# Performance work log

Measured on AMD Instinct MI355X. Metric: run time of the kernel, lower is better.

The kernel has to match this reference:

```python
import jax, jax.numpy as jnp
import numpy as np

SEQ, B, IN, HID = 512, 64, 1024, 1024


def setup_inputs() -> dict:
    key = jax.random.key(0)
    ks = jax.random.split(key, 9)
    scale = 1.0 / np.sqrt(IN + HID)  # ~torch Linear init range
    def lin(k):
        kw, kb = jax.random.split(k)
        W = jax.random.uniform(kw, (IN + HID, HID), jnp.float32, -scale, scale)
        b = jax.random.uniform(kb, (HID,), jnp.float32, -scale, scale)
        return W, b
    W_f, b_f = lin(ks[0])
    W_i, b_i = lin(ks[1])
    W_o, b_o = lin(ks[2])
    W_c, b_c = lin(ks[3])
    x = jax.random.normal(ks[4], (SEQ, B, IN), jnp.float32)
    return {"x": x, "W_f": W_f, "b_f": b_f, "W_i": W_i, "b_i": b_i,
            "W_o": W_o, "b_o": b_o, "W_c": W_c, "b_c": b_c}


def reference(x, W_f, b_f, W_i, b_i, W_o, b_o, W_c, b_c):
    # x: [seq, batch, input_size]; z = concat(hidden, x_t) to match torch.cat((hidden, input[j]), 1)
    batch = x.shape[1]
    hid = W_f.shape[1]
    h0 = jnp.zeros((batch, hid), x.dtype)
    c0 = jnp.zeros((batch, hid), x.dtype)

    def step(carry, xt):
        h, c = carry
        z = jnp.concatenate([h, xt], axis=1)          # [B, hid+in]
        f = jax.nn.sigmoid(z @ W_f + b_f)
        i = jax.nn.sigmoid(z @ W_i + b_i)
        o = jax.nn.sigmoid(z @ W_o + b_o)
        C_hat = jnp.tanh(z @ W_c + b_c)
        c = c * f + C_hat * i
        h = jnp.tanh(c) * o
        return (h, c), h

    (h, c), output = jax.lax.scan(step, (h0, c0), x)  # output: [seq, B, hid]
    return output, h, c
```

## Files before the change

kernel.cpp:

```cpp
#include <hip/hip_runtime.h>
#include <hip/hip_bf16.h>


typedef __attribute__((ext_vector_type(8))) short short8;
typedef __attribute__((ext_vector_type(4))) float f32x4;
typedef __attribute__((ext_vector_type(4))) unsigned int u32x4;

#define SEQ  512
#define NBAT 64
#define RING 128

static __device__ __forceinline__ unsigned short f2b(float f) {
  unsigned u = __float_as_uint(f);
  unsigned r = (u + 0x7fffu + ((u >> 16) & 1u)) >> 16;
  return (unsigned short)r;
}

static __device__ __forceinline__ void gld_lds16(const void* g, void* l) {
  __builtin_amdgcn_global_load_lds((const __attribute__((address_space(1))) void*)g,
                                   (__attribute__((address_space(3))) void*)l, 16, 0, 0);
}
static __device__ __forceinline__ void gld_lds16_sc1(const void* g, void* l) {
  __builtin_amdgcn_global_load_lds((const __attribute__((address_space(1))) void*)g,
                                   (__attribute__((address_space(3))) void*)l, 16, 0, 16);
}

static __device__ __forceinline__ float sigf(float x) { return 1.f / (1.f + __expf(-x)); }
static __device__ __forceinline__ float tanhfast(float x) { return 1.f - 2.f / (1.f + __expf(2.f * x)); }


__global__ __launch_bounds__(512) void pack_w(const float* __restrict__ Wf,
                                              const float* __restrict__ Wi,
                                              const float* __restrict__ Wo,
                                              const float* __restrict__ Wc,
                                              unsigned short* __restrict__ Wht,
                                              unsigned short* __restrict__ Wxt) {
  __shared__ float tile[64][65];
  int bx = blockIdx.x;
  int g  = bx & 3; bx >>= 2;
  int jb = bx & 15;
  int kb = bx >> 4;
  int j0 = jb * 64, k0 = kb * 64;
  const float* W = (g == 0) ? Wf : (g == 1) ? Wi : (g == 2) ? Wo : Wc;
  int t = threadIdx.x;
  {
    int r  = t >> 3;
    int c0 = (t & 7) * 8;
    const float* src = W + (size_t)(k0 + r) * 1024 + j0 + c0;
    float4 a = *(const float4*)src;
    float4 b = *(const float4*)(src + 4);
    tile[r][c0 + 0] = a.x; tile[r][c0 + 1] = a.y; tile[r][c0 + 2] = a.z; tile[r][c0 + 3] = a.w;
    tile[r][c0 + 4] = b.x; tile[r][c0 + 5] = b.y; tile[r][c0 + 6] = b.z; tile[r][c0 + 7] = b.w;
  }
  __syncthreads();
  {
    int jj  = t >> 3;
    int cc8 = t & 7;
    unsigned short v[8];
#pragma unroll
    for (int e = 0; e < 8; ++e) v[e] = f2b(tile[cc8 * 8 + e][jj]);
    size_t p = (size_t)(4 * (j0 + jj) + g);
    if (k0 < 1024)
      *(uint4*)(&Wht[p * 1024 + k0 + cc8 * 8]) = *(const uint4*)v;
    else
      *(uint4*)(&Wxt[p * 1024 + (k0 - 1024) + cc8 * 8]) = *(const uint4*)v;
  }
}

__global__ __launch_bounds__(256) void pack_bias(const float* __restrict__ bf,
                                                 const float* __restrict__ bi,
                                                 const float* __restrict__ bo,
                                                 const float* __restrict__ bc,
                                                 float* __restrict__ bp) {
  int p = blockIdx.x * 256 + threadIdx.x;
  if (p < 4096) {
    int j = p >> 2, g = p & 3;
    const float* b = (g == 0) ? bf : (g == 1) ? bi : (g == 2) ? bo : bc;
    bp[p] = b[j];
  }
}

__global__ __launch_bounds__(256) void conv_x(const float* __restrict__ x,
                                              unsigned short* __restrict__ xb, int n8) {
  int i = blockIdx.x * 256 + threadIdx.x;
  if (i < n8) {
    const float4* xp = (const float4*)x + (size_t)i * 2;
    float4 a = xp[0], b = xp[1];
    unsigned short v[8] = {f2b(a.x), f2b(a.y), f2b(a.z), f2b(a.w),
                           f2b(b.x), f2b(b.y), f2b(b.z), f2b(b.w)};
    *(uint4*)(&xb[(size_t)i * 8]) = *(const uint4*)v;
  }
}

__global__ __launch_bounds__(256) void init_state(unsigned short* __restrict__ hA,
                                                  float* __restrict__ c,
                                                  int* __restrict__ flags,
                                                  int* __restrict__ gxcnt) {
  int i = blockIdx.x * 256 + threadIdx.x;
  if (i < NBAT * 1024) { hA[i] = 0; c[i] = 0.f; }
  if (i < 128) flags[i] = 0;
  if (i < 256) gxcnt[i] = 0;
}


__global__ __launch_bounds__(256, 1) void lstm_fused(
    const unsigned short* __restrict__ Wht,
    const unsigned short* __restrict__ Wxt,
    const float* __restrict__ bp,
    const unsigned short* __restrict__ xb,
    float* __restrict__ GxRing,
    unsigned short* __restrict__ hA,
    unsigned short* __restrict__ hB,
    float* __restrict__ cst,
    float* __restrict__ out,
    float* __restrict__ outH,
    float* __restrict__ outC,
    int* __restrict__ flags,
    int* __restrict__ gxcnt) {
  __shared__ __align__(16) char lds[139584];

  const int tid = threadIdx.x;
  const int bid = blockIdx.x;
  const int lane = tid & 63;

  if (bid < 128) {
    unsigned short* Ws = (unsigned short*)lds;
    char*           Ab = lds + 65536;
    float (*G)[33]     = (float(*)[33])(lds + 131072);
    int* tok           = (int*)(lds + 139520);

    const int w   = tid >> 6;
    const int w16 = w * 16;
    const int rl  = lane & 15;
    const int kb  = lane >> 4;
    const int p0  = bid * 32;

    {
      const unsigned short* Wsrc = Wht + (size_t)p0 * 1024;
#pragma unroll
      for (int r = 0; r < 16; ++r) {
        int s = r * 256 + tid;
        int row = s >> 7;
        int slot = s & 127;
        int sub = (slot & 7) ^ (row & 7);
        gld_lds16(Wsrc + (size_t)row * 1024 + ((slot & ~7) | sub) * 8,
                  Ws + (size_t)(r * 256 + (tid & 192)) * 8);
      }
    }

    const int gb   = tid >> 2;
    const int gjl  = (tid & 3) * 2;
    const int gidx = gb * 1024 + (p0 >> 2) + gjl;
    float c0 = cst[gidx], c1 = cst[gidx + 1];

    if (tid == 0) *tok = 0;
    asm volatile("s_waitcnt vmcnt(0)" ::: "memory");
    __syncthreads();

#define ASTAGE(c_)                                                             \
    {                                                                          \
      const unsigned short* hrow = hsrc + (size_t)w16 * 1024 + (c_) * 128;     \
      char* dbase = Ab + ((c_) & 3) * 16384 + w * 4096;                        \
      _Pragma("unroll") for (int i = 0; i < 4; ++i) {                          \
        int s = i * 64 + lane;                                                 \
        int row_loc = s >> 4;                                                  \
        int slot = s & 15;                                                     \
        int src = slot ^ (row_loc & 7);                                        \
        gld_lds16_sc1(hrow + (size_t)row_loc * 1024 + src * 8,                 \
                      dbase + i * 1024);                                       \
      }                                                                        \
    }

    for (int t = 0; t < SEQ; ++t) {
      const unsigned short* hsrc = (t & 1) ? hB : hA;
      unsigned int*         hdst = (unsigned int*)((t & 1) ? hA : hB);

      if (w == 0) {
        int cready = __hip_atomic_load(&gxcnt[t >> 1], __ATOMIC_RELAXED, __HIP_MEMORY_SCOPE_AGENT);
        if (t > 0) {
          while (true) {
            int m0 = __hip_atomic_load(&flags[lane * 2],     __ATOMIC_RELAXED, __HIP_MEMORY_SCOPE_AGENT);
            int m1 = __hip_atomic_load(&flags[lane * 2 + 1], __ATOMIC_RELAXED, __HIP_MEMORY_SCOPE_AGENT);
            if (__all(m0 >= t && m1 >= t)) break;
            __builtin_amdgcn_s_sleep(1);
          }
        }
        if (cready < 32) {
          while (__hip_atomic_load(&gxcnt[t >> 1], __ATOMIC_RELAXED, __HIP_MEMORY_SCOPE_AGENT) < 32)
            __builtin_amdgcn_s_sleep(2);
        }
        __hip_atomic_store(tok, t + 1, __ATOMIC_RELAXED, __HIP_MEMORY_SCOPE_WORKGROUP);
      } else {
        while (__hip_atomic_load(tok, __ATOMIC_RELAXED, __HIP_MEMORY_SCOPE_WORKGROUP) < t + 1) {
        }
      }
      __builtin_amdgcn_sched_barrier(0);

      u32x4 gxa, gxb;
      {
        const float* gsrc = GxRing + (size_t)(t & (RING - 1)) * 262144 +
                            (size_t)gb * 4096 + p0 + gjl * 4;
        asm volatile("global_load_dwordx4 %0, %1, off sc1" : "=v"(gxa) : "v"(gsrc));
        asm volatile("global_load_dwordx4 %0, %1, off offset:16 sc1" : "=v"(gxb) : "v"(gsrc));
      }
      __builtin_amdgcn_sched_barrier(0);

      ASTAGE(0); ASTAGE(1); ASTAGE(2); ASTAGE(3);

      f32x4 acc0 = (f32x4){0.f, 0.f, 0.f, 0.f};
      f32x4 acc1 = (f32x4){0.f, 0.f, 0.f, 0.f};

#pragma unroll
      for (int kc = 0; kc < 8; ++kc) {
        if      (kc <= 4) asm volatile("s_waitcnt vmcnt(12)" ::: "memory");
        else if (kc == 5) asm volatile("s_waitcnt vmcnt(8)"  ::: "memory");
        else if (kc == 6) asm volatile("s_waitcnt vmcnt(4)"  ::: "memory");
        else              asm volatile("s_waitcnt vmcnt(0)"  ::: "memory");
        __builtin_amdgcn_sched_barrier(0);
        const char* Abc = Ab + (kc & 3) * 16384 + w * 4096;
#pragma unroll
        for (int ks = 0; ks < 4; ++ks) {
          int g = ks * 4 + kb;
          short8 af = *(const short8*)(Abc + rl * 256 + ((g ^ (rl & 7)) * 16));
          int gslot = kc * 16 + g;
          int gbase = (gslot & ~7) * 16;
          short8 bf0 = *(const short8*)((const char*)Ws + (0 * 16 + rl) * 2048 + gbase +
                                        (((gslot & 7) ^ (rl & 7)) * 16));
          short8 bf1 = *(const short8*)((const char*)Ws + (1 * 16 + rl) * 2048 + gbase +
                                        (((gslot & 7) ^ (rl & 7)) * 16));
          acc0 = __builtin_amdgcn_mfma_f32_16x16x32_bf16(af, bf0, acc0, 0, 0, 0);
          acc1 = __builtin_amdgcn_mfma_f32_16x16x32_bf16(af, bf1, acc1, 0, 0, 0);
        }
        if (kc + 4 < 8) ASTAGE(kc + 4);
      }

#pragma unroll
      for (int r = 0; r < 4; ++r) {
        G[w16 + kb * 4 + r][rl]      = acc0[r];
        G[w16 + kb * 4 + r][16 + rl] = acc1[r];
      }
      f32x4 gx0 = __builtin_bit_cast(f32x4, gxa);
      f32x4 gx1 = __builtin_bit_cast(f32x4, gxb);
      float f0 = sigf(G[gb][gjl * 4 + 0] + gx0[0]);
      float i0 = sigf(G[gb][gjl * 4 + 1] + gx0[1]);
      float o0 = sigf(G[gb][gjl * 4 + 2] + gx0[2]);
      float q0 = tanhfast(G[gb][gjl * 4 + 3] + gx0[3]);
      float f1 = sigf(G[gb][gjl * 4 + 4] + gx1[0]);
      float i1 = sigf(G[gb][gjl * 4 + 5] + gx1[1]);
      float o1 = sigf(G[gb][gjl * 4 + 6] + gx1[2]);
      float q1 = tanhfast(G[gb][gjl * 4 + 7] + gx1[3]);
      c0 = c0 * f0 + q0 * i0;
      c1 = c1 * f1 + q1 * i1;
      float h0 = tanhfast(c0) * o0;
      float h1 = tanhfast(c1) * o1;

      __hip_atomic_store(&hdst[gidx >> 1],
                         ((unsigned)f2b(h1) << 16) | (unsigned)f2b(h0),
                         __ATOMIC_RELAXED, __HIP_MEMORY_SCOPE_AGENT);
      asm volatile("s_waitcnt vmcnt(0)" ::: "memory");
      __syncthreads();
      if (tid == 0)
        __hip_atomic_store(&flags[bid], t + 1, __ATOMIC_RELAXED, __HIP_MEMORY_SCOPE_AGENT);

      *(float2*)&out[(size_t)t * 65536 + gidx] = make_float2(h0, h1);
      if (t == SEQ - 1) {
        *(float2*)&outH[gidx] = make_float2(h0, h1);
        *(float2*)&outC[gidx] = make_float2(c0, c1);
      }
    }
#undef ASTAGE

    cst[gidx]     = c0;
    cst[gidx + 1] = c1;

  } else {
    unsigned short* AsW = (unsigned short*)lds;
    unsigned short* BsW = (unsigned short*)(lds + 32768);
    const int wid = bid - 128;
    const int w = tid >> 6;
    const int rl = lane & 15, kb = lane >> 4;
    const int wr = w >> 1, wc = w & 1;

    for (int tau = wid; tau < 8192; tau += 128) {
      int sp = tau >> 5;
      int bn = tau & 31;

      if (2 * sp >= RING - 16) {
        int need = 2 * sp - (RING - 16) + 1;
        while (__hip_atomic_load(&flags[0], __ATOMIC_RELAXED, __HIP_MEMORY_SCOPE_AGENT) < need)
          __builtin_amdgcn_s_sleep(16);
      }

      const unsigned short* Abase = xb + (size_t)sp * 131072;
      const unsigned short* Bbase = Wxt + (size_t)bn * 131072;

      f32x4 acc[4][4];
#pragma unroll
      for (int m = 0; m < 4; ++m)
#pragma unroll
        for (int n = 0; n < 4; ++n) acc[m][n] = (f32x4){0.f, 0.f, 0.f, 0.f};

#define GSTAGE(k0_, buf_)                                                       \
      {                                                                         \
        _Pragma("unroll") for (int r = 0; r < 4; ++r) {                         \
          int i = r * 256 + tid;                                                \
          int row = i >> 3;                                                     \
          int cc = (i & 7) ^ (row & 7);                                         \
          int base = (r * 256 + (tid & 192)) * 8;                               \
          gld_lds16(Abase + (size_t)row * 1024 + (k0_) + cc * 8, &AsW[(buf_)*8192 + base]); \
          gld_lds16(Bbase + (size_t)row * 1024 + (k0_) + cc * 8, &BsW[(buf_)*8192 + base]); \
        }                                                                       \
      }

      GSTAGE(0, 0);
      __syncthreads();
      int cur = 0;
#pragma unroll 2
      for (int kc = 0; kc < 16; ++kc) {
        if (kc < 15) GSTAGE((kc + 1) * 64, cur ^ 1);
        const char* Abt = (const char*)&AsW[cur * 8192];
        const char* Bbt = (const char*)&BsW[cur * 8192];
#pragma unroll
        for (int ks = 0; ks < 2; ++ks) {
          int g = ks * 4 + kb;
          short8 bf[4], af[4];
#pragma unroll
          for (int nt = 0; nt < 4; ++nt) {
            int brow = wc * 64 + nt * 16 + rl;
            bf[nt] = *(const short8*)(Bbt + brow * 128 + ((g ^ (brow & 7)) * 16));
          }
#pragma unroll
          for (int mt = 0; mt < 4; ++mt) {
            int arow = wr * 64 + mt * 16 + rl;
            af[mt] = *(const short8*)(Abt + arow * 128 + ((g ^ (arow & 7)) * 16));
          }
#pragma unroll
          for (int mt = 0; mt < 4; ++mt)
#pragma unroll
            for (int nt = 0; nt < 4; ++nt)
              acc[mt][nt] = __builtin_amdgcn_mfma_f32_16x16x32_bf16(af[mt], bf[nt], acc[mt][nt], 0, 0, 0);
        }
        __syncthreads();
        cur ^= 1;
      }
#undef GSTAGE

      float* Cb = GxRing + (size_t)((2 * sp) & (RING - 1)) * 262144;
#pragma unroll
      for (int nt = 0; nt < 4; ++nt) {
        int p = bn * 128 + wc * 64 + nt * 16 + rl;
        float bias = bp[p];
#pragma unroll
        for (int mt = 0; mt < 4; ++mt) {
#pragma unroll
          for (int r = 0; r < 4; ++r) {
            int row = wr * 64 + mt * 16 + kb * 4 + r;
            __hip_atomic_store(&Cb[(size_t)row * 4096 + p], acc[mt][nt][r] + bias,
                               __ATOMIC_RELAXED, __HIP_MEMORY_SCOPE_AGENT);
          }
        }
      }
      asm volatile("s_waitcnt vmcnt(0)" ::: "memory");
      __syncthreads();
      if (tid == 0)
        __hip_atomic_fetch_add(&gxcnt[sp], 1, __ATOMIC_RELAXED, __HIP_MEMORY_SCOPE_AGENT);
    }
  }
}


extern "C" void kernel_launch(void* const* d_in, const int* in_sizes, int n_in,
                              void* d_out, int out_size, void* d_ws, size_t ws_size,
                              hipStream_t stream) {
  const float* x  = (const float*)d_in[0];
  const float* Wf = (const float*)d_in[1];
  const float* bf = (const float*)d_in[2];
  const float* Wi = (const float*)d_in[3];
  const float* bi = (const float*)d_in[4];
  const float* Wo = (const float*)d_in[5];
  const float* bo = (const float*)d_in[6];
  const float* Wc = (const float*)d_in[7];
  const float* bc = (const float*)d_in[8];
  float* out = (float*)d_out;

  char* ws = (char*)d_ws;
  unsigned short* Wht = (unsigned short*)(ws);
  unsigned short* Wxt = (unsigned short*)(ws + 8388608);
  float*          bp  = (float*)(ws + 16777216);
  unsigned short* xb  = (unsigned short*)(ws + 16793600);
  unsigned short* hA  = (unsigned short*)(ws + 83902464);
  unsigned short* hB  = (unsigned short*)(ws + 84033536);
  float*          cst = (float*)(ws + 84164608);
  int*            flg = (int*)(ws + 84426752);
  int*            gxc = (int*)(ws + 84430848);
  float*          GxR = (float*)(ws + 84440064);

  pack_w    <<<2048,  512, 0, stream>>>(Wf, Wi, Wo, Wc, Wht, Wxt);
  pack_bias <<<16,    256, 0, stream>>>(bf, bi, bo, bc, bp);
  conv_x    <<<16384, 256, 0, stream>>>(x, xb, 4194304);
  init_state<<<256,   256, 0, stream>>>(hA, cst, flg, gxc);

  float* outH = out + (size_t)SEQ * NBAT * 1024;
  float* outC = outH + NBAT * 1024;

  lstm_fused<<<256, 256, 0, stream>>>(Wht, Wxt, bp, xb, GxR, hA, hB, cst,
                                      out, outH, outC, flg, gxc);
}
```

Measured before the change: 3.203 ms.

## Replace flag/counter barriers with sentinel-poisoned data polling in LSTM recurrence

```diff
diff --git a/kernel.cpp b/kernel.cpp
--- a/kernel.cpp
+++ b/kernel.cpp
@@ -8,7 +8,7 @@
 
 #define SEQ  512
 #define NBAT 64
-#define RING 128
+#define RING 32
 
 static __device__ __forceinline__ unsigned short f2b(float f) {
   unsigned u = __float_as_uint(f);
@@ -19,10 +19,6 @@
 static __device__ __forceinline__ void gld_lds16(const void* g, void* l) {
   __builtin_amdgcn_global_load_lds((const __attribute__((address_space(1))) void*)g,
                                    (__attribute__((address_space(3))) void*)l, 16, 0, 0);
-}
-static __device__ __forceinline__ void gld_lds16_sc1(const void* g, void* l) {
-  __builtin_amdgcn_global_load_lds((const __attribute__((address_space(1))) void*)g,
-                                   (__attribute__((address_space(3))) void*)l, 16, 0, 16);
 }
 
 static __device__ __forceinline__ float sigf(float x) { return 1.f / (1.f + __expf(-x)); }
@@ -92,14 +88,19 @@
   }
 }
 
-__global__ __launch_bounds__(256) void init_state(unsigned short* __restrict__ hA,
+__global__ __launch_bounds__(256) void init_state(unsigned int* __restrict__ hR,
                                                   float* __restrict__ c,
-                                                  int* __restrict__ flags,
-                                                  int* __restrict__ gxcnt) {
+                                                  int* __restrict__ flags) {
   int i = blockIdx.x * 256 + threadIdx.x;
-  if (i < NBAT * 1024) { hA[i] = 0; c[i] = 0.f; }
+  if (i < 131072) hR[i] = (i < 98304) ? ~0u : 0u;
+  if (i < 65536) c[i] = 0.f;
   if (i < 128) flags[i] = 0;
-  if (i < 256) gxcnt[i] = 0;
+}
+
+__global__ __launch_bounds__(256) void fill_ring(u32x4* __restrict__ g, int n4) {
+  u32x4 nan4; nan4[0] = ~0u; nan4[1] = ~0u; nan4[2] = ~0u; nan4[3] = ~0u;
+  for (int k = blockIdx.x * 256 + threadIdx.x; k < n4; k += 524288)
+    g[k] = nan4;
 }
 
 
@@ -109,14 +110,12 @@
     const float* __restrict__ bp,
     const unsigned short* __restrict__ xb,
     float* __restrict__ GxRing,
-    unsigned short* __restrict__ hA,
-    unsigned short* __restrict__ hB,
+    unsigned short* __restrict__ hR,
     float* __restrict__ cst,
     float* __restrict__ out,
     float* __restrict__ outH,
     float* __restrict__ outC,
-    int* __restrict__ flags,
-    int* __restrict__ gxcnt) {
+    int* __restrict__ flags) {
   __shared__ __align__(16) char lds[139584];
 
   const int tid = threadIdx.x;
@@ -127,7 +126,6 @@
     unsigned short* Ws = (unsigned short*)lds;
     char*           Ab = lds + 65536;
     float (*G)[33]     = (float(*)[33])(lds + 131072);
-    int* tok           = (int*)(lds + 139520);
 
     const int w   = tid >> 6;
     const int w16 = w * 16;
@@ -153,70 +151,97 @@
     const int gidx = gb * 1024 + (p0 >> 2) + gjl;
     float c0 = cst[gidx], c1 = cst[gidx + 1];
 
-    if (tid == 0) *tok = 0;
     asm volatile("s_waitcnt vmcnt(0)" ::: "memory");
     __syncthreads();
 
-#define ASTAGE(c_)                                                             \
-    {                                                                          \
-      const unsigned short* hrow = hsrc + (size_t)w16 * 1024 + (c_) * 128;     \
-      char* dbase = Ab + ((c_) & 3) * 16384 + w * 4096;                        \
-      _Pragma("unroll") for (int i = 0; i < 4; ++i) {                          \
-        int s = i * 64 + lane;                                                 \
-        int row_loc = s >> 4;                                                  \
-        int slot = s & 15;                                                     \
-        int src = slot ^ (row_loc & 7);                                        \
-        gld_lds16_sc1(hrow + (size_t)row_loc * 1024 + src * 8,                 \
-                      dbase + i * 1024);                                       \
-      }                                                                        \
-    }
+    const int klane = lane >> 4;
+    const int sl    = lane & 15;
+    const int x0 = klane * 2048 + ((sl ^ klane) * 16);
+    const int x1 = (4 + klane) * 2048 + (((sl ^ klane) ^ 4) * 16);
+    const int x2 = x0 + 16384;
+    const int x3 = x1 + 16384;
+    const int wb = w * 32768;
+    char* AbW = Ab + w * 4096 + (size_t)lane * 16;
+
+    const int c_own = bid >> 4;
+    const int ocg   = bid & 15;
+    const int own0  = ((sl ^ klane) == ocg);
+    const int own1  = ((sl ^ (klane + 4)) == ocg);
+    const int row_loc_own = gb - w16;
+    char* ownlds = Ab + (c_own & 3) * 16384 + w * 4096 +
+                   (row_loc_own * 16 + (ocg ^ (row_loc_own & 7))) * 16 + (tid & 3) * 4;
+
+    unsigned hp_prev = 0;
+
+#define HISSUE(c_)                                                             \
+    { const char* cb_ = hbase + (c_) * 256;                                    \
+      asm volatile("global_load_dwordx4 %0, %1, off sc0 sc1"                   \
+                   : "=v"(ch[(c_) & 3][0]) : "v"(cb_ + x0));                   \
+      asm volatile("global_load_dwordx4 %0, %1, off sc0 sc1"                   \
+                   : "=v"(ch[(c_) & 3][1]) : "v"(cb_ + x1));                   \
+      asm volatile("global_load_dwordx4 %0, %1, off sc0 sc1"                   \
+                   : "=v"(ch[(c_) & 3][2]) : "v"(cb_ + x2));                   \
+      asm volatile("global_load_dwordx4 %0, %1, off sc0 sc1"                   \
+                   : "=v"(ch[(c_) & 3][3]) : "v"(cb_ + x3)); }
+
+#define KWAIT(kc_)                                                             \
+    { if ((kc_) <= 4)      asm volatile("s_waitcnt vmcnt(12)" ::: "memory");   \
+      else if ((kc_) == 5) asm volatile("s_waitcnt vmcnt(8)"  ::: "memory");   \
+      else if ((kc_) == 6) asm volatile("s_waitcnt vmcnt(4)"  ::: "memory");   \
+      else                 asm volatile("s_waitcnt vmcnt(0)"  ::: "memory"); }
 
     for (int t = 0; t < SEQ; ++t) {
-      const unsigned short* hsrc = (t & 1) ? hB : hA;
-      unsigned int*         hdst = (unsigned int*)((t & 1) ? hA : hB);
-
-      if (w == 0) {
-        int cready = __hip_atomic_load(&gxcnt[t >> 1], __ATOMIC_RELAXED, __HIP_MEMORY_SCOPE_AGENT);
-        if (t > 0) {
-          while (true) {
-            int m0 = __hip_atomic_load(&flags[lane * 2],     __ATOMIC_RELAXED, __HIP_MEMORY_SCOPE_AGENT);
-            int m1 = __hip_atomic_load(&flags[lane * 2 + 1], __ATOMIC_RELAXED, __HIP_MEMORY_SCOPE_AGENT);
-            if (__all(m0 >= t && m1 >= t)) break;
-            __builtin_amdgcn_s_sleep(1);
-          }
-        }
-        if (cready < 32) {
-          while (__hip_atomic_load(&gxcnt[t >> 1], __ATOMIC_RELAXED, __HIP_MEMORY_SCOPE_AGENT) < 32)
-            __builtin_amdgcn_s_sleep(2);
-        }
-        __hip_atomic_store(tok, t + 1, __ATOMIC_RELAXED, __HIP_MEMORY_SCOPE_WORKGROUP);
-      } else {
-        while (__hip_atomic_load(tok, __ATOMIC_RELAXED, __HIP_MEMORY_SCOPE_WORKGROUP) < t + 1) {
-        }
-      }
+      const char*   hbase = (const char*)hR + ((t + 3) & 3) * 131072 + wb;
+      unsigned int* hdst  = (unsigned int*)((char*)hR + (t & 3) * 131072);
+      unsigned int* hwip  = (unsigned int*)((char*)hR + ((t + 2) & 3) * 131072);
+      float* gsrc = GxRing + (size_t)(t & (RING - 1)) * 262144 +
+                    (size_t)gb * 4096 + p0 + gjl * 4;
+
+      u32x4 gxa, gxb;
+      asm volatile("global_load_dwordx4 %0, %1, off sc0 sc1" : "=v"(gxa) : "v"(gsrc));
+      asm volatile("global_load_dwordx4 %0, %1, off offset:16 sc0 sc1" : "=v"(gxb) : "v"(gsrc));
+      u32x4 ch[4][4];
+      HISSUE(0); HISSUE(1); HISSUE(2); HISSUE(3);
       __builtin_amdgcn_sched_barrier(0);
-
-      u32x4 gxa, gxb;
-      {
-        const float* gsrc = GxRing + (size_t)(t & (RING - 1)) * 262144 +
-                            (size_t)gb * 4096 + p0 + gjl * 4;
-        asm volatile("global_load_dwordx4 %0, %1, off sc1" : "=v"(gxa) : "v"(gsrc));
-        asm volatile("global_load_dwordx4 %0, %1, off offset:16 sc1" : "=v"(gxb) : "v"(gsrc));
-      }
-      __builtin_amdgcn_sched_barrier(0);
-
-      ASTAGE(0); ASTAGE(1); ASTAGE(2); ASTAGE(3);
 
       f32x4 acc0 = (f32x4){0.f, 0.f, 0.f, 0.f};
       f32x4 acc1 = (f32x4){0.f, 0.f, 0.f, 0.f};
 
 #pragma unroll
       for (int kc = 0; kc < 8; ++kc) {
-        if      (kc <= 4) asm volatile("s_waitcnt vmcnt(12)" ::: "memory");
-        else if (kc == 5) asm volatile("s_waitcnt vmcnt(8)"  ::: "memory");
-        else if (kc == 6) asm volatile("s_waitcnt vmcnt(4)"  ::: "memory");
-        else              asm volatile("s_waitcnt vmcnt(0)"  ::: "memory");
+        KWAIT(kc);
         __builtin_amdgcn_sched_barrier(0);
+
+        int rtry = 0;
+        for (;;) {
+          int s0, s1, s2, s3;
+          { u32x4 v = ch[kc & 3][0]; s0 = (v[0]==~0u)|(v[1]==~0u)|(v[2]==~0u)|(v[3]==~0u); }
+          { u32x4 v = ch[kc & 3][1]; s1 = (v[0]==~0u)|(v[1]==~0u)|(v[2]==~0u)|(v[3]==~0u); }
+          { u32x4 v = ch[kc & 3][2]; s2 = (v[0]==~0u)|(v[1]==~0u)|(v[2]==~0u)|(v[3]==~0u); }
+          { u32x4 v = ch[kc & 3][3]; s3 = (v[0]==~0u)|(v[1]==~0u)|(v[2]==~0u)|(v[3]==~0u); }
+          if (kc == c_own) { s0 &= !own0; s1 &= !own1; s2 &= !own0; s3 &= !own1; }
+          if (!__any(s0 | s1 | s2 | s3) || ++rtry > 2048) break;
+          asm volatile("s_waitcnt vmcnt(0)" ::: "memory");
+          __builtin_amdgcn_sched_barrier(0);
+          __builtin_amdgcn_s_sleep(4);
+          HISSUE(kc);
+          asm volatile("s_waitcnt vmcnt(0)" ::: "memory");
+          __builtin_amdgcn_sched_barrier(0);
+        }
+        if (rtry) {
+          if (kc + 1 < 8) HISSUE(kc + 1);
+          if (kc + 2 < 8) HISSUE(kc + 2);
+          if (kc + 3 < 8) HISSUE(kc + 3);
+        }
+
+        { char* wA = AbW + (kc & 3) * 16384;
+          *(u32x4*)(wA)          = ch[kc & 3][0];
+          *(u32x4*)(wA + 1024)   = ch[kc & 3][1];
+          *(u32x4*)(wA + 2048)   = ch[kc & 3][2];
+          *(u32x4*)(wA + 3072)   = ch[kc & 3][3]; }
+        if (kc == c_own) *(unsigned*)ownlds = hp_prev;
+        if (kc + 4 < 8) HISSUE(kc + 4);
+
         const char* Abc = Ab + (kc & 3) * 16384 + w * 4096;
 #pragma unroll
         for (int ks = 0; ks < 4; ++ks) {
@@ -231,7 +256,6 @@
           acc0 = __builtin_amdgcn_mfma_f32_16x16x32_bf16(af, bf0, acc0, 0, 0, 0);
           acc1 = __builtin_amdgcn_mfma_f32_16x16x32_bf16(af, bf1, acc1, 0, 0, 0);
         }
-        if (kc + 4 < 8) ASTAGE(kc + 4);
       }
 
 #pragma unroll
@@ -239,6 +263,21 @@
         G[w16 + kb * 4 + r][rl]      = acc0[r];
         G[w16 + kb * 4 + r][16 + rl] = acc1[r];
       }
+
+      {
+        int spin = 0;
+        for (;;) {
+          int bad = (gxa[0]==~0u)|(gxa[1]==~0u)|(gxa[2]==~0u)|(gxa[3]==~0u)|
+                    (gxb[0]==~0u)|(gxb[1]==~0u)|(gxb[2]==~0u)|(gxb[3]==~0u);
+          if (!__any(bad) || ++spin > 4096) break;
+          __builtin_amdgcn_s_sleep(4);
+          asm volatile("global_load_dwordx4 %0, %1, off sc0 sc1" : "=v"(gxa) : "v"(gsrc));
+          asm volatile("global_load_dwordx4 %0, %1, off offset:16 sc0 sc1" : "=v"(gxb) : "v"(gsrc));
+          asm volatile("s_waitcnt vmcnt(0)" ::: "memory");
+          __builtin_amdgcn_sched_barrier(0);
+        }
+      }
+
       f32x4 gx0 = __builtin_bit_cast(f32x4, gxa);
       f32x4 gx1 = __builtin_bit_cast(f32x4, gxb);
       float f0 = sigf(G[gb][gjl * 4 + 0] + gx0[0]);
@@ -254,10 +293,17 @@
       float h0 = tanhfast(c0) * o0;
       float h1 = tanhfast(c1) * o1;
 
-      __hip_atomic_store(&hdst[gidx >> 1],
-                         ((unsigned)f2b(h1) << 16) | (unsigned)f2b(h0),
-                         __ATOMIC_RELAXED, __HIP_MEMORY_SCOPE_AGENT);
-      asm volatile("s_waitcnt vmcnt(0)" ::: "memory");
+      unsigned hp = ((unsigned)f2b(h1) << 16) | (unsigned)f2b(h0);
+      __hip_atomic_store(&hdst[gidx >> 1], hp, __ATOMIC_RELAXED, __HIP_MEMORY_SCOPE_AGENT);
+      hp_prev = hp;
+
+      { u32x4 nan4; nan4[0] = ~0u; nan4[1] = ~0u; nan4[2] = ~0u; nan4[3] = ~0u;
+        asm volatile("global_store_dwordx4 %0, %1, off sc0 sc1"
+                     :: "v"(gsrc), "v"(nan4) : "memory");
+        asm volatile("global_store_dwordx4 %0, %1, off offset:16 sc0 sc1"
+                     :: "v"(gsrc), "v"(nan4) : "memory"); }
+      __hip_atomic_store(&hwip[gidx >> 1], ~0u, __ATOMIC_RELAXED, __HIP_MEMORY_SCOPE_AGENT);
+
       __syncthreads();
       if (tid == 0)
         __hip_atomic_store(&flags[bid], t + 1, __ATOMIC_RELAXED, __HIP_MEMORY_SCOPE_AGENT);
@@ -268,7 +314,8 @@
         *(float2*)&outC[gidx] = make_float2(c0, c1);
       }
     }
-#undef ASTAGE
+#undef HISSUE
+#undef KWAIT
 
     cst[gidx]     = c0;
     cst[gidx + 1] = c1;
@@ -362,8 +409,6 @@
       }
       asm volatile("s_waitcnt vmcnt(0)" ::: "memory");
       __syncthreads();
-      if (tid == 0)
-        __hip_atomic_fetch_add(&gxcnt[sp], 1, __ATOMIC_RELAXED, __HIP_MEMORY_SCOPE_AGENT);
     }
   }
 }
@@ -388,21 +433,20 @@
   unsigned short* Wxt = (unsigned short*)(ws + 8388608);
   float*          bp  = (float*)(ws + 16777216);
   unsigned short* xb  = (unsigned short*)(ws + 16793600);
-  unsigned short* hA  = (unsigned short*)(ws + 83902464);
-  unsigned short* hB  = (unsigned short*)(ws + 84033536);
-  float*          cst = (float*)(ws + 84164608);
-  int*            flg = (int*)(ws + 84426752);
-  int*            gxc = (int*)(ws + 84430848);
-  float*          GxR = (float*)(ws + 84440064);
+  unsigned short* hRp = (unsigned short*)(ws + 83902464);
+  float*          cst = (float*)(ws + 84426752);
+  int*            flg = (int*)(ws + 84688896);
+  float*          GxR = (float*)(ws + 84692992);
 
   pack_w    <<<2048,  512, 0, stream>>>(Wf, Wi, Wo, Wc, Wht, Wxt);
   pack_bias <<<16,    256, 0, stream>>>(bf, bi, bo, bc, bp);
   conv_x    <<<16384, 256, 0, stream>>>(x, xb, 4194304);
-  init_state<<<256,   256, 0, stream>>>(hA, cst, flg, gxc);
+  init_state<<<512,   256, 0, stream>>>((unsigned int*)hRp, cst, flg);
+  fill_ring <<<2048,  256, 0, stream>>>((u32x4*)GxR, 2097152);
 
   float* outH = out + (size_t)SEQ * NBAT * 1024;
   float* outC = outH + NBAT * 1024;
 
-  lstm_fused<<<256, 256, 0, stream>>>(Wht, Wxt, bp, xb, GxR, hA, hB, cst,
-                                      out, outH, outC, flg, gxc);
-}
+  lstm_fused<<<256, 256, 0, stream>>>(Wht, Wxt, bp, xb, GxR, hRp, cst,
+                                      out, outH, outC, flg);
+}
```

New measurement: 3.638 ms. 1.14x slower.

## Replace per-block step barrier with per-wave flags for recurrent LSTM sync

Applied to the files above, without the earlier changes.

```diff
diff --git a/kernel.cpp b/kernel.cpp
--- a/kernel.cpp
+++ b/kernel.cpp
@@ -94,12 +94,14 @@
 
 __global__ __launch_bounds__(256) void init_state(unsigned short* __restrict__ hA,
                                                   float* __restrict__ c,
-                                                  int* __restrict__ flags,
-                                                  int* __restrict__ gxcnt) {
+                                                  int* __restrict__ flagw,
+                                                  int* __restrict__ gxcnt,
+                                                  int* __restrict__ flags4) {
   int i = blockIdx.x * 256 + threadIdx.x;
   if (i < NBAT * 1024) { hA[i] = 0; c[i] = 0.f; }
-  if (i < 128) flags[i] = 0;
+  if (i < 512) flagw[i] = 0;
   if (i < 256) gxcnt[i] = 0;
+  if (i < 4)   flags4[i] = 0;
 }
 
 
@@ -115,8 +117,9 @@
     float* __restrict__ out,
     float* __restrict__ outH,
     float* __restrict__ outC,
-    int* __restrict__ flags,
-    int* __restrict__ gxcnt) {
+    int* __restrict__ flagw,
+    int* __restrict__ gxcnt,
+    int* __restrict__ flags4) {
   __shared__ __align__(16) char lds[139584];
 
   const int tid = threadIdx.x;
@@ -127,7 +130,6 @@
     unsigned short* Ws = (unsigned short*)lds;
     char*           Ab = lds + 65536;
     float (*G)[33]     = (float(*)[33])(lds + 131072);
-    int* tok           = (int*)(lds + 139520);
 
     const int w   = tid >> 6;
     const int w16 = w * 16;
@@ -153,9 +155,10 @@
     const int gidx = gb * 1024 + (p0 >> 2) + gjl;
     float c0 = cst[gidx], c1 = cst[gidx + 1];
 
-    if (tid == 0) *tok = 0;
     asm volatile("s_waitcnt vmcnt(0)" ::: "memory");
     __syncthreads();
+
+    const int fbase = w * 128;
 
 #define ASTAGE(c_)                                                             \
     {                                                                          \
@@ -175,23 +178,13 @@
       const unsigned short* hsrc = (t & 1) ? hB : hA;
       unsigned int*         hdst = (unsigned int*)((t & 1) ? hA : hB);
 
-      if (w == 0) {
-        int cready = __hip_atomic_load(&gxcnt[t >> 1], __ATOMIC_RELAXED, __HIP_MEMORY_SCOPE_AGENT);
-        if (t > 0) {
-          while (true) {
-            int m0 = __hip_atomic_load(&flags[lane * 2],     __ATOMIC_RELAXED, __HIP_MEMORY_SCOPE_AGENT);
-            int m1 = __hip_atomic_load(&flags[lane * 2 + 1], __ATOMIC_RELAXED, __HIP_MEMORY_SCOPE_AGENT);
-            if (__all(m0 >= t && m1 >= t)) break;
-            __builtin_amdgcn_s_sleep(1);
-          }
-        }
-        if (cready < 32) {
-          while (__hip_atomic_load(&gxcnt[t >> 1], __ATOMIC_RELAXED, __HIP_MEMORY_SCOPE_AGENT) < 32)
-            __builtin_amdgcn_s_sleep(2);
-        }
-        __hip_atomic_store(tok, t + 1, __ATOMIC_RELAXED, __HIP_MEMORY_SCOPE_WORKGROUP);
-      } else {
-        while (__hip_atomic_load(tok, __ATOMIC_RELAXED, __HIP_MEMORY_SCOPE_WORKGROUP) < t + 1) {
+      {
+        while (true) {
+          int m0 = __hip_atomic_load(&flagw[fbase + lane * 2],     __ATOMIC_RELAXED, __HIP_MEMORY_SCOPE_AGENT);
+          int m1 = __hip_atomic_load(&flagw[fbase + lane * 2 + 1], __ATOMIC_RELAXED, __HIP_MEMORY_SCOPE_AGENT);
+          int cg = __hip_atomic_load(&gxcnt[t >> 1],               __ATOMIC_RELAXED, __HIP_MEMORY_SCOPE_AGENT);
+          if (__all((m0 >= t) && (m1 >= t) && (cg >= 32))) break;
+          __builtin_amdgcn_s_sleep(1);
         }
       }
       __builtin_amdgcn_sched_barrier(0);
@@ -258,15 +251,18 @@
                          ((unsigned)f2b(h1) << 16) | (unsigned)f2b(h0),
                          __ATOMIC_RELAXED, __HIP_MEMORY_SCOPE_AGENT);
       asm volatile("s_waitcnt vmcnt(0)" ::: "memory");
-      __syncthreads();
-      if (tid == 0)
-        __hip_atomic_store(&flags[bid], t + 1, __ATOMIC_RELAXED, __HIP_MEMORY_SCOPE_AGENT);
+      if (lane == 0) {
+        __hip_atomic_store(&flagw[fbase + bid], t + 1, __ATOMIC_RELAXED, __HIP_MEMORY_SCOPE_AGENT);
+        if (bid == 0)
+          __hip_atomic_store(&flags4[w], t + 1, __ATOMIC_RELAXED, __HIP_MEMORY_SCOPE_AGENT);
+      }
 
       *(float2*)&out[(size_t)t * 65536 + gidx] = make_float2(h0, h1);
       if (t == SEQ - 1) {
         *(float2*)&outH[gidx] = make_float2(h0, h1);
         *(float2*)&outC[gidx] = make_float2(c0, c1);
       }
+      asm volatile("s_waitcnt vmcnt(0)" ::: "memory");
     }
 #undef ASTAGE
 
@@ -287,8 +283,11 @@
 
       if (2 * sp >= RING - 16) {
         int need = 2 * sp - (RING - 16) + 1;
-        while (__hip_atomic_load(&flags[0], __ATOMIC_RELAXED, __HIP_MEMORY_SCOPE_AGENT) < need)
+        while (true) {
+          int v = __hip_atomic_load(&flags4[lane & 3], __ATOMIC_RELAXED, __HIP_MEMORY_SCOPE_AGENT);
+          if (__all(v >= need)) break;
           __builtin_amdgcn_s_sleep(16);
+        }
       }
 
       const unsigned short* Abase = xb + (size_t)sp * 131072;
@@ -391,18 +390,19 @@
   unsigned short* hA  = (unsigned short*)(ws + 83902464);
   unsigned short* hB  = (unsigned short*)(ws + 84033536);
   float*          cst = (float*)(ws + 84164608);
-  int*            flg = (int*)(ws + 84426752);
+  int*            flw = (int*)(ws + 84426752);
   int*            gxc = (int*)(ws + 84430848);
+  int*            fl4 = (int*)(ws + 84431872);
   float*          GxR = (float*)(ws + 84440064);
 
   pack_w    <<<2048,  512, 0, stream>>>(Wf, Wi, Wo, Wc, Wht, Wxt);
   pack_bias <<<16,    256, 0, stream>>>(bf, bi, bo, bc, bp);
   conv_x    <<<16384, 256, 0, stream>>>(x, xb, 4194304);
-  init_state<<<256,   256, 0, stream>>>(hA, cst, flg, gxc);
+  init_state<<<256,   256, 0, stream>>>(hA, cst, flw, gxc, fl4);
 
   float* outH = out + (size_t)SEQ * NBAT * 1024;
   float* outC = outH + NBAT * 1024;
 
   lstm_fused<<<256, 256, 0, stream>>>(Wht, Wxt, bp, xb, GxR, hA, hB, cst,
-                                      out, outH, outC, flg, gxc);
-}
+                                      out, outH, outC, flw, gxc, fl4);
+}
```

Result: faster. 2.867 ms, median of 3 (-10.5%).
